# Kernel optimization log

Measured on AMD Instinct MI355X. Metric: run time of the kernel, lower is better.

## Reference

```python
import jax, jax.numpy as jnp
import numpy as np

# DSCNPair config (init_kwargs)
C = 256          # d_model
G = 16           # group
K = 3            # kernel_size
DW = 3           # dw_kernel_size
PAD = 1
STRIDE = 1
DIL = 1
GC = C // G      # group_channels
P = K * K        # sampling points per group
OFFSET_SCALE = 1.0
B, H, W = 8, 64, 64


def _dwconv(x, w, b, pad):
    # depthwise conv: x (N,C,H,W), w (C,1,kh,kw)
    out = jax.lax.conv_general_dilated(
        x, w, (1, 1), [(pad, pad), (pad, pad)],
        dimension_numbers=('NCHW', 'OIHW', 'NCHW'), feature_group_count=x.shape[1])
    return out + b[None, :, None, None]


def _dcn_core(x, offset, mask):
    # x: (N,H,W,C) NHWC; offset: (N,H,W,G*P*2); mask: (N,H,W,G*P) already softmaxed per group
    N, Hh, Ww, _ = x.shape
    xp = jnp.pad(x, ((0, 0), (PAD, PAD), (PAD, PAD), (0, 0)))
    Hp, Wp = Hh + 2 * PAD, Ww + 2 * PAD
    Ho = (Hp - (DIL * (K - 1) + 1)) // STRIDE + 1
    Wo = (Wp - (DIL * (K - 1) + 1)) // STRIDE + 1
    # reference points (normalized by padded spatial size)
    base = (DIL * (K - 1)) // 2 + 0.5
    ref_y = (base + jnp.arange(Ho, dtype=x.dtype) * STRIDE) / Hp
    ref_x = (base + jnp.arange(Wo, dtype=x.dtype) * STRIDE) / Wp
    # dilation grid, kw-major ordering to match torch.meshgrid(lin_w, lin_h) in DCNv3
    pts = -((DIL * (K - 1)) // 2) + jnp.arange(K, dtype=x.dtype) * DIL
    gx = jnp.repeat(pts, K) / Wp
    gy = jnp.tile(pts, K) / Hp
    off = offset.reshape(N, Ho, Wo, G, P, 2) * (OFFSET_SCALE / jnp.array([Wp, Hp], x.dtype))
    loc_x = ref_x[None, None, :, None, None] + OFFSET_SCALE * gx + off[..., 0]  # (N,Ho,Wo,G,P)
    loc_y = ref_y[None, :, None, None, None] + OFFSET_SCALE * gy + off[..., 1]
    # grid_sample(bilinear, padding_mode='zeros', align_corners=False):
    # grid g = 2*loc-1; unnormalized idx = ((g+1)*size - 1)/2 = loc*size - 0.5
    ix = loc_x * Wp - 0.5
    iy = loc_y * Hp - 0.5
    x0 = jnp.floor(ix)
    y0 = jnp.floor(iy)
    xg = xp.reshape(N, Hp, Wp, G, GC)
    n_idx = jnp.arange(N)[:, None, None, None, None]
    g_idx = jnp.arange(G)[None, None, None, :, None]

    def gather(yi, xi):
        valid = ((yi >= 0) & (yi < Hp) & (xi >= 0) & (xi < Wp)).astype(x.dtype)
        yc = jnp.clip(yi, 0, Hp - 1).astype(jnp.int32)
        xc = jnp.clip(xi, 0, Wp - 1).astype(jnp.int32)
        return xg[n_idx, yc, xc, g_idx] * valid[..., None]  # (N,Ho,Wo,G,P,GC)

    wx1 = ix - x0; wx0 = 1.0 - wx1
    wy1 = iy - y0; wy0 = 1.0 - wy1
    out = (gather(y0, x0) * (wy0 * wx0)[..., None]
           + gather(y0, x0 + 1) * (wy0 * wx1)[..., None]
           + gather(y0 + 1, x0) * (wy1 * wx0)[..., None]
           + gather(y0 + 1, x0 + 1) * (wy1 * wx1)[..., None])
    out = (out * mask.reshape(N, Ho, Wo, G, P, 1)).sum(4)   # (N,Ho,Wo,G,GC)
    return out.reshape(N, Ho, Wo, G * GC)


def _forward(x, conv0_w, conv0_b, dw_w, dw_b, ln_g, ln_b, off_w, off_b,
             msk_w, msk_b, in_w, in_b, outp_w, outp_b, pw_w, pw_b):
    u = x
    h = _dwconv(x, conv0_w, conv0_b, 2)             # 5x5 depthwise, pad 2
    inp = jnp.transpose(h, (0, 2, 3, 1))            # NHWC, input to DCNv3
    xproj = inp @ in_w + in_b                       # input_proj
    # dw_conv branch: depthwise conv -> LayerNorm(channels_last) -> GELU
    x1 = _dwconv(jnp.transpose(inp, (0, 3, 1, 2)), dw_w, dw_b, (DW - 1) // 2)
    x1 = jnp.transpose(x1, (0, 2, 3, 1))
    mu = x1.mean(-1, keepdims=True)
    var = jnp.mean((x1 - mu) ** 2, -1, keepdims=True)
    x1 = (x1 - mu) * jax.lax.rsqrt(var + 1e-5) * ln_g + ln_b
    x1 = jax.nn.gelu(x1, approximate=False)
    offset = x1 @ off_w + off_b                     # (B,H,W,G*P*2)
    m = jax.nn.softmax((x1 @ msk_w + msk_b).reshape(B, H, W, G, P), axis=-1)
    m = m.reshape(B, H, W, G * P)
    y = _dcn_core(xproj, offset, m)
    y = y @ outp_w + outp_b                         # output_proj
    attn = jnp.einsum('nhwc,dc->ndhw', y, pw_w) + pw_b[None, :, None, None]  # 1x1 conv
    return u * attn


def setup_inputs() -> dict:
    key = jax.random.key(0)
    ks = jax.random.split(key, 8)
    s = 0.05
    return {
        'x': jax.random.normal(ks[0], (B, C, H, W), jnp.float32),
        'conv0_w': jax.random.normal(ks[1], (C, 1, 5, 5), jnp.float32) * s,
        'conv0_b': jnp.zeros((C,), jnp.float32),
        'dw_w': jax.random.normal(ks[2], (C, 1, DW, DW), jnp.float32) * s,
        'dw_b': jnp.zeros((C,), jnp.float32),
        'ln_g': jnp.ones((C,), jnp.float32),
        'ln_b': jnp.zeros((C,), jnp.float32),
        'off_w': jax.random.normal(ks[3], (C, G * P * 2), jnp.float32) * s,
        'off_b': jnp.zeros((G * P * 2,), jnp.float32),
        'msk_w': jax.random.normal(ks[4], (C, G * P), jnp.float32) * s,
        'msk_b': jnp.zeros((G * P,), jnp.float32),
        'in_w': jax.random.normal(ks[5], (C, C), jnp.float32) * s,
        'in_b': jnp.zeros((C,), jnp.float32),
        'outp_w': jax.random.normal(ks[6], (C, C), jnp.float32) * s,
        'outp_b': jnp.zeros((C,), jnp.float32),
        'pw_w': jax.random.normal(ks[7], (C, C), jnp.float32) * s,
        'pw_b': jnp.zeros((C,), jnp.float32),
    }


def reference(x, conv0_w, conv0_b, dw_w, dw_b, ln_g, ln_b, off_w, off_b,
              msk_w, msk_b, in_w, in_b, outp_w, outp_b, pw_w, pw_b):
    return _forward(x, conv0_w, conv0_b, dw_w, dw_b, ln_g, ln_b, off_w, off_b,
                    msk_w, msk_b, in_w, in_b, outp_w, outp_b, pw_w, pw_b)
```

## Files before the change

kernel.cpp:

```cpp
#include <hip/hip_runtime.h>
#include <hip/hip_bf16.h>
#include <hip/hip_fp16.h>
#include <math.h>

#define BB 8
#define CC 256
#define HH 64
#define WW 64
#define GG 16
#define GCH 16
#define PP 9
#define NPIX (BB*HH*WW)

typedef __attribute__((ext_vector_type(4))) float f32x4;
typedef __bf16 bf16x8 __attribute__((ext_vector_type(8)));

#define GLOAD_LDS16(g, l) __builtin_amdgcn_global_load_lds( \
    (const __attribute__((address_space(1))) unsigned int*)(g), \
    (__attribute__((address_space(3))) unsigned int*)(l), 16, 0, 0)

__device__ __forceinline__ void bfu2(unsigned a, float& lo, float& hi) {
    union { unsigned u; float f; } t0, t1;
    t0.u = a << 16; t1.u = a & 0xffff0000u;
    lo = t0.f; hi = t1.f;
}

#define C0PLANE 817
__global__ void conv0_kernel(const float* __restrict__ x, const float* __restrict__ w,
                             const float* __restrict__ b,
                             __hip_bfloat16* __restrict__ out_bf) {
    __shared__ float sx[16 * C0PLANE];
    int t  = threadIdx.x;
    int st = blockIdx.x;
    int cg = blockIdx.y;
    int n  = blockIdx.z;
    int h0 = st * 8;
    int c0 = cg * 16;

    #pragma unroll
    for (int i = 0; i < 12; ++i) {
        int task = i * 256 + t;
        int lane = task & 15;
        int pair = task >> 4;
        int c    = pair / 12;
        int row  = pair - c * 12;
        int gy   = h0 - 2 + row;
        float4 v = make_float4(0.f, 0.f, 0.f, 0.f);
        if (gy >= 0 && gy < HH)
            v = *(const float4*)(x + (((size_t)(n * CC + c0 + c)) * HH + gy) * WW + lane * 4);
        *(float4*)&sx[c * C0PLANE + row * 68 + 2 + lane * 4] = v;
    }
    if (t < 192) {
        int c = t / 12, row = t - (t / 12) * 12;
        float* p = &sx[c * C0PLANE + row * 68];
        p[0] = 0.f; p[1] = 0.f; p[66] = 0.f; p[67] = 0.f;
    }
    __syncthreads();

    int c = t & 15;
    int s = t >> 4;
    float wreg[25];
    const float* wp = w + (c0 + c) * 25;
    #pragma unroll
    for (int i = 0; i < 25; ++i) wreg[i] = wp[i];
    float bias = b[c0 + c];
    const float* cp = &sx[c * C0PLANE + s * 4];

    float win[5][8];
    #pragma unroll
    for (int rr = 0; rr < 4; ++rr)
        #pragma unroll
        for (int j = 0; j < 8; ++j) win[rr][j] = cp[rr * 68 + j];

    #pragma unroll
    for (int r = 0; r < 8; ++r) {
        #pragma unroll
        for (int j = 0; j < 8; ++j) win[(r + 4) % 5][j] = cp[(r + 4) * 68 + j];
        float a0 = bias, a1 = bias, a2 = bias, a3 = bias;
        #pragma unroll
        for (int dy = 0; dy < 5; ++dy) {
            const float* wr = &wreg[dy * 5];
            const float* wd = win[(r + dy) % 5];
            #pragma unroll
            for (int dx = 0; dx < 5; ++dx) {
                float wv = wr[dx];
                a0 += wd[0 + dx] * wv;
                a1 += wd[1 + dx] * wv;
                a2 += wd[2 + dx] * wv;
                a3 += wd[3 + dx] * wv;
            }
        }
        size_t pixb = ((size_t)n * 4096 + (h0 + r) * 64 + s * 4) << 8;
        out_bf[pixb + c0 + c]       = __float2bfloat16(a0);
        out_bf[pixb + 256 + c0 + c] = __float2bfloat16(a1);
        out_bf[pixb + 512 + c0 + c] = __float2bfloat16(a2);
        out_bf[pixb + 768 + c0 + c] = __float2bfloat16(a3);
    }
}

__global__ void dwln_kernel(const __hip_bfloat16* __restrict__ inp, const float* __restrict__ dww,
                            const float* __restrict__ dwb, const float* __restrict__ lng,
                            const float* __restrict__ lnb, __hip_bfloat16* __restrict__ x1) {
    __shared__ float sx[3 * 10 * 256];
    __shared__ float ls1[8][4], ls2[8][4];
    int t  = threadIdx.x;
    int x0 = blockIdx.x * 8;
    int h  = blockIdx.y;
    int n  = blockIdx.z;

    #pragma unroll
    for (int i = 0; i < 4; ++i) {
        int task = i * 256 + t;
        if (task < 960) {
            int c8  = task & 31;
            int rem = task >> 5;
            int r   = rem / 10;
            int xx  = rem - r * 10;
            int gy = h + r - 1, gx = x0 + xx - 1;
            float4 A = make_float4(0.f,0.f,0.f,0.f), B = make_float4(0.f,0.f,0.f,0.f);
            if (gy >= 0 && gy < HH && gx >= 0 && gx < WW) {
                uint4 u = *(const uint4*)(inp + (((size_t)(n * HH + gy)) * WW + gx) * CC + c8 * 8);
                bfu2(u.x, A.x, A.y); bfu2(u.y, A.z, A.w);
                bfu2(u.z, B.x, B.y); bfu2(u.w, B.z, B.w);
            }
            *(float4*)&sx[(r * 10 + xx) * 256 + c8 * 8]     = A;
            *(float4*)&sx[(r * 10 + xx) * 256 + c8 * 8 + 4] = B;
        }
    }
    __syncthreads();

    int c = t;
    float wr[9];
    #pragma unroll
    for (int i = 0; i < 9; ++i) wr[i] = dww[c * 9 + i];
    float bias = dwb[c];
    float a[8];
    #pragma unroll
    for (int px = 0; px < 8; ++px) {
        float acc = bias;
        #pragma unroll
        for (int dy = 0; dy < 3; ++dy)
            #pragma unroll
            for (int dx = 0; dx < 3; ++dx)
                acc += sx[(dy * 10 + px + dx) * 256 + c] * wr[dy * 3 + dx];
        a[px] = acc;
    }

    int wid = t >> 6, lane = t & 63;
    #pragma unroll
    for (int px = 0; px < 8; ++px) {
        float s1 = a[px], s2 = a[px] * a[px];
        #pragma unroll
        for (int o = 1; o < 64; o <<= 1) {
            s1 += __shfl_xor(s1, o);
            s2 += __shfl_xor(s2, o);
        }
        if (lane == 0) { ls1[px][wid] = s1; ls2[px][wid] = s2; }
    }
    __syncthreads();

    float gam = lng[c], bet = lnb[c];
    #pragma unroll
    for (int px = 0; px < 8; ++px) {
        float t1 = ls1[px][0] + ls1[px][1] + ls1[px][2] + ls1[px][3];
        float t2 = ls2[px][0] + ls2[px][1] + ls2[px][2] + ls2[px][3];
        float mu  = t1 * (1.0f/256.0f);
        float var = t2 * (1.0f/256.0f) - mu * mu;
        float rr  = rsqrtf(var + 1e-5f);
        float v = (a[px] - mu) * rr * gam + bet;
        float g = 0.5f * v * (1.0f + erff(v * 0.70710678118654752440f));
        x1[(((size_t)(n * HH + h)) * WW + x0 + px) * CC + c] = __float2bfloat16(g);
    }
}

__global__ void wcvt_t_kernel(const float* __restrict__ W, __hip_bfloat16* __restrict__ Bt, int N) {
    int idx = blockIdx.x * 256 + threadIdx.x;
    int n = idx >> 8, k = idx & 255;
    float v = (n < N) ? W[k * N + n] : 0.0f;
    Bt[idx] = __float2bfloat16(v);
}
__global__ void wcomb_kernel(const float* __restrict__ outpw, const float* __restrict__ pww,
                             __hip_bfloat16* __restrict__ Wc) {
    __shared__ float pd[256];
    int d = blockIdx.x, k = threadIdx.x;
    pd[k] = pww[d * 256 + k];
    __syncthreads();
    const float* ow = outpw + k * 256;
    float s = 0.0f;
    #pragma unroll 8
    for (int c = 0; c < 256; ++c) s += ow[c] * pd[c];
    Wc[d * 256 + k] = __float2bfloat16(s);
}
__global__ void bcomb_kernel(const float* __restrict__ outpb, const float* __restrict__ pww,
                             const float* __restrict__ pwb, float* __restrict__ bc) {
    int d = threadIdx.x;
    const float* pr = pww + d * 256;
    float s = pwb[d];
    #pragma unroll 8
    for (int c = 0; c < 256; ++c) s += outpb[c] * pr[c];
    bc[d] = s;
}

__device__ __forceinline__ void stage_tile(const __hip_bfloat16* __restrict__ A,
                                           const __hip_bfloat16* __restrict__ Bt,
                                           __bf16* As, __bf16* Bs,
                                           int bm, int bn, int k0, int w, int l) {
    #pragma unroll
    for (int i = 0; i < 4; ++i) {
        int q = w*256 + i*64 + l;
        int row = q >> 3, sk = q & 7;
        const __hip_bfloat16* g = A + (((size_t)(bm + row)) << 8) + k0 + sk*8;
        GLOAD_LDS16(g, As + (w*256 + i*64)*8);
    }
    #pragma unroll
    for (int i = 0; i < 2; ++i) {
        int q = w*128 + i*64 + l;
        int row = q >> 3, sk = q & 7;
        const __hip_bfloat16* g = Bt + (((size_t)(bn + row)) << 8) + k0 + sk*8;
        GLOAD_LDS16(g, Bs + (w*128 + i*64)*8);
    }
}

template <int OUT_BF16, int NBOUND>
__global__ void mgemm_kernel(const __hip_bfloat16* __restrict__ A,
                             const __hip_bfloat16* __restrict__ Bt,
                             const float* __restrict__ bias,
                             void* __restrict__ Cout, int N, int ldc) {
    __shared__ __bf16 smem[24576];
    int tid = threadIdx.x;
    int w = tid >> 6, l = tid & 63;
    int bn = blockIdx.x * 64;
    int bm = blockIdx.y * 128;
    __bf16* Asb[2] = { smem,        smem + 12288 };
    __bf16* Bsb[2] = { smem + 8192, smem + 20480 };
    f32x4 acc[2][4];
    #pragma unroll
    for (int m = 0; m < 2; ++m)
        #pragma unroll
        for (int n = 0; n < 4; ++n)
            acc[m][n] = (f32x4){0.f, 0.f, 0.f, 0.f};

    stage_tile(A, Bt, Asb[0], Bsb[0], bm, bn, 0, w, l);
    __syncthreads();
    int lr = l & 15, kg = l >> 4;
    #pragma unroll
    for (int t = 0; t < 4; ++t) {
        int cur = t & 1;
        if (t < 3) stage_tile(A, Bt, Asb[cur^1], Bsb[cur^1], bm, bn, (t+1)*64, w, l);
        const __bf16* Ab = Asb[cur];
        const __bf16* Bb = Bsb[cur];
        bf16x8 af[2][2], bfr[4][2];
        #pragma unroll
        for (int m = 0; m < 2; ++m)
            #pragma unroll
            for (int u = 0; u < 2; ++u)
                af[m][u] = *(const bf16x8*)&Ab[(w*32 + m*16 + lr)*64 + u*32 + kg*8];
        #pragma unroll
        for (int n = 0; n < 4; ++n)
            #pragma unroll
            for (int u = 0; u < 2; ++u)
                bfr[n][u] = *(const bf16x8*)&Bb[(n*16 + lr)*64 + u*32 + kg*8];
        #pragma unroll
        for (int u = 0; u < 2; ++u)
            #pragma unroll
            for (int m = 0; m < 2; ++m)
                #pragma unroll
                for (int n = 0; n < 4; ++n)
                    acc[m][n] = __builtin_amdgcn_mfma_f32_16x16x32_bf16(af[m][u], bfr[n][u], acc[m][n], 0, 0, 0);
        __syncthreads();
    }
    int orow = bm + w*32 + kg*4;
    #pragma unroll
    for (int n = 0; n < 4; ++n) {
        int ccol = bn + n*16 + lr;
        if (NBOUND && ccol >= N) continue;
        float bv = bias[ccol];
        #pragma unroll
        for (int m = 0; m < 2; ++m) {
            #pragma unroll
            for (int j = 0; j < 4; ++j) {
                size_t o = (size_t)(orow + m*16 + j) * ldc + ccol;
                float v = acc[m][n][j] + bv;
                if (OUT_BF16) ((__hip_bfloat16*)Cout)[o] = __float2bfloat16(v);
                else          ((float*)Cout)[o] = v;
            }
        }
    }
}

__global__ void dcn_kernel(const __hip_bfloat16* __restrict__ xproj,
                           const __hip_bfloat16* __restrict__ off,
                           const __hip_bfloat16* __restrict__ mlog,
                           __hip_bfloat16* __restrict__ y) {
    __shared__ uint2 wLds[1152];
    __shared__ int   oLds[1152];
    int pix0 = blockIdx.x * 8;
    int t = threadIdx.x;

    if (t < 128) {
        int px = t >> 4;
        int g  = t & 15;
        int pix = pix0 + px;
        int wo = pix & 63, ho = (pix >> 6) & 63;
        const __hip_bfloat16* mb = mlog + (size_t)pix * 144 + g * 9;
        float lg[9];
        float mx = -1e30f;
        #pragma unroll
        for (int p = 0; p < 9; ++p) { lg[p] = __bfloat162float(mb[p]); mx = fmaxf(mx, lg[p]); }
        float se = 0.f;
        #pragma unroll
        for (int p = 0; p < 9; ++p) { lg[p] = __expf(lg[p] - mx); se += lg[p]; }
        float rs = 1.0f / se;
        const unsigned* ob = (const unsigned*)(off + (size_t)pix * 288 + g * 18);
        #pragma unroll
        for (int p = 0; p < 9; ++p) {
            float ox, oy;
            bfu2(ob[p], ox, oy);
            float m = lg[p] * rs;
            int dx = p / 3 - 1;
            int dy = p - (p / 3) * 3 - 1;
            float fx = (float)(wo + dx) + ox;
            float fy = (float)(ho + dy) + oy;
            float x0f = floorf(fx), y0f = floorf(fy);
            int x0 = (int)x0f, y0 = (int)y0f;
            int x1 = x0 + 1, y1 = y0 + 1;
            float wx1 = fx - x0f, wx0 = 1.0f - wx1;
            float wy1 = fy - y0f, wy0 = 1.0f - wy1;
            float vx0 = (x0 >= 0 && x0 < WW) ? 1.0f : 0.0f;
            float vx1 = (x1 >= 0 && x1 < WW) ? 1.0f : 0.0f;
            float vy0 = (y0 >= 0 && y0 < HH) ? 1.0f : 0.0f;
            float vy1 = (y1 >= 0 && y1 < HH) ? 1.0f : 0.0f;
            int x0c = min(max(x0, 0), WW - 1), x1c = min(max(x1, 0), WW - 1);
            int y0c = min(max(y0, 0), HH - 1), y1c = min(max(y1, 0), HH - 1);
            int tau = px * 144 + g * 9 + p;
            union { __half2 h2; unsigned u; } pa, pb;
            pa.h2 = __floats2half2_rn(m * wy0 * wx0 * vy0 * vx0,
                                      m * wy0 * wx1 * vy0 * vx1);
            pb.h2 = __floats2half2_rn(m * wy1 * wx0 * vy1 * vx0,
                                      m * wy1 * wx1 * vy1 * vx1);
            wLds[tau] = make_uint2(pa.u, pb.u);
            oLds[tau] = (y0c * WW + x0c) | ((x1c - x0c) << 12) | ((y1c - y0c) << 13);
        }
    }
    __syncthreads();

    int px = t >> 5;
    int l  = t & 31;
    int g  = l >> 1;
    int ch = g * 16 + (l & 1) * 8;
    int pix = pix0 + px;
    int n = pix >> 12;
    const __hip_bfloat16* xb = xproj + ((size_t)n << 20) + ch;
    float a0=0,a1=0,a2=0,a3=0,a4=0,a5=0,a6=0,a7=0;
    const uint2* wp = &wLds[px * 144 + g * 9];
    const int*   op = &oLds[px * 144 + g * 9];
    #pragma unroll
    for (int p = 0; p < 9; ++p) {
        uint2 pw = wp[p];
        union { unsigned u; __half2 h2; } ua, ub;
        ua.u = pw.x; ub.u = pw.y;
        float2 fA = __half22float2(ua.h2);
        float2 fB = __half22float2(ub.h2);
        float w00 = fA.x, w01 = fA.y, w10 = fB.x, w11 = fB.y;
        int pk = op[p];
        int base = (pk & 4095) << 8;
        int ddx  = ((pk >> 12) & 1) << 8;
        int ddy  = ((pk >> 13) & 1) << 14;
        {
            uint4 u = *(const uint4*)(xb + base);
            float b0,b1,b2,b3,b4,b5,b6,b7;
            bfu2(u.x,b0,b1); bfu2(u.y,b2,b3); bfu2(u.z,b4,b5); bfu2(u.w,b6,b7);
            a0 += w00*b0; a1 += w00*b1; a2 += w00*b2; a3 += w00*b3;
            a4 += w00*b4; a5 += w00*b5; a6 += w00*b6; a7 += w00*b7;
        }
        {
            uint4 u = *(const uint4*)(xb + base + ddx);
            float b0,b1,b2,b3,b4,b5,b6,b7;
            bfu2(u.x,b0,b1); bfu2(u.y,b2,b3); bfu2(u.z,b4,b5); bfu2(u.w,b6,b7);
            a0 += w01*b0; a1 += w01*b1; a2 += w01*b2; a3 += w01*b3;
            a4 += w01*b4; a5 += w01*b5; a6 += w01*b6; a7 += w01*b7;
        }
        {
            uint4 u = *(const uint4*)(xb + base + ddy);
            float b0,b1,b2,b3,b4,b5,b6,b7;
            bfu2(u.x,b0,b1); bfu2(u.y,b2,b3); bfu2(u.z,b4,b5); bfu2(u.w,b6,b7);
            a0 += w10*b0; a1 += w10*b1; a2 += w10*b2; a3 += w10*b3;
            a4 += w10*b4; a5 += w10*b5; a6 += w10*b6; a7 += w10*b7;
        }
        {
            uint4 u = *(const uint4*)(xb + base + ddy + ddx);
            float b0,b1,b2,b3,b4,b5,b6,b7;
            bfu2(u.x,b0,b1); bfu2(u.y,b2,b3); bfu2(u.z,b4,b5); bfu2(u.w,b6,b7);
            a0 += w11*b0; a1 += w11*b1; a2 += w11*b2; a3 += w11*b3;
            a4 += w11*b4; a5 += w11*b5; a6 += w11*b6; a7 += w11*b7;
        }
    }
    union { __hip_bfloat16 h[8]; uint4 u; } ov;
    ov.h[0]=__float2bfloat16(a0); ov.h[1]=__float2bfloat16(a1);
    ov.h[2]=__float2bfloat16(a2); ov.h[3]=__float2bfloat16(a3);
    ov.h[4]=__float2bfloat16(a4); ov.h[5]=__float2bfloat16(a5);
    ov.h[6]=__float2bfloat16(a6); ov.h[7]=__float2bfloat16(a7);
    *(uint4*)(y + (size_t)pix * CC + ch) = ov.u;
}

__global__ void finmul_kernel(const float* __restrict__ x, const __hip_bfloat16* __restrict__ attn,
                              float* __restrict__ out) {
    __shared__ float t[16][17];
    int pix0 = blockIdx.x * 16;
    int d0   = blockIdx.y * 16;
    int li = threadIdx.x & 15;
    int lj = threadIdx.x >> 4;
    t[lj][li] = __bfloat162float(attn[(size_t)(pix0 + lj)*CC + d0 + li]);
    __syncthreads();
    int pix = pix0 + li;
    int wo = pix & 63;
    int ho = (pix >> 6) & 63;
    int n  = pix >> 12;
    int d = d0 + lj;
    size_t oidx = (((size_t)n*CC + d)*HH + ho)*WW + wo;
    out[oidx] = x[oidx] * t[li][lj];
}

extern "C" void kernel_launch(void* const* d_in, const int* in_sizes, int n_in,
                              void* d_out, int out_size, void* d_ws, size_t ws_size,
                              hipStream_t stream) {
    const float* x      = (const float*)d_in[0];
    const float* conv0w = (const float*)d_in[1];
    const float* conv0b = (const float*)d_in[2];
    const float* dww    = (const float*)d_in[3];
    const float* dwb    = (const float*)d_in[4];
    const float* lng    = (const float*)d_in[5];
    const float* lnb    = (const float*)d_in[6];
    const float* offw   = (const float*)d_in[7];
    const float* offb   = (const float*)d_in[8];
    const float* mskw   = (const float*)d_in[9];
    const float* mskb   = (const float*)d_in[10];
    const float* inw    = (const float*)d_in[11];
    const float* inb    = (const float*)d_in[12];
    const float* outpw  = (const float*)d_in[13];
    const float* outpb  = (const float*)d_in[14];
    const float* pww    = (const float*)d_in[15];
    const float* pwb    = (const float*)d_in[16];

    __hip_bfloat16* bfb = (__hip_bfloat16*)d_ws;
    __hip_bfloat16* inp_bf  = bfb;
    __hip_bfloat16* y_bf    = inp_bf;
    __hip_bfloat16* x1_bf   = bfb + 8388608;
    __hip_bfloat16* xpj_bf  = x1_bf;
    __hip_bfloat16* attn_bf = x1_bf;
    __hip_bfloat16* off_bf  = bfb + 16777216;
    __hip_bfloat16* msk_bf  = bfb + 26214400;
    __hip_bfloat16* bt_in   = bfb + 30932992;
    __hip_bfloat16* bt_off  = bt_in  + 65536;
    __hip_bfloat16* bt_msk  = bt_off + 81920;
    __hip_bfloat16* bt_wc   = bt_msk + 49152;
    float* bcomb = (float*)(bt_wc + 65536);
    float* out = (float*)d_out;

    wcvt_t_kernel<<<256, 256, 0, stream>>>(inw,  bt_in,  256);
    wcvt_t_kernel<<<320, 256, 0, stream>>>(offw, bt_off, 288);
    wcvt_t_kernel<<<192, 256, 0, stream>>>(mskw, bt_msk, 144);
    wcomb_kernel<<<256, 256, 0, stream>>>(outpw, pww, bt_wc);
    bcomb_kernel<<<1, 256, 0, stream>>>(outpb, pww, pwb, bcomb);

    conv0_kernel<<<dim3(8, 16, BB), 256, 0, stream>>>(x, conv0w, conv0b, inp_bf);
    dwln_kernel<<<dim3(8, 64, BB), 256, 0, stream>>>(inp_bf, dww, dwb, lng, lnb, x1_bf);
    mgemm_kernel<1,1><<<dim3(5, 256), 256, 0, stream>>>(x1_bf, bt_off, offb, off_bf, 288, 288);
    mgemm_kernel<1,1><<<dim3(3, 256), 256, 0, stream>>>(x1_bf, bt_msk, mskb, msk_bf, 144, 144);
    mgemm_kernel<1,0><<<dim3(4, 256), 256, 0, stream>>>(inp_bf, bt_in, inb, xpj_bf, 256, 256);
    dcn_kernel<<<NPIX/8, 256, 0, stream>>>(xpj_bf, off_bf, msk_bf, y_bf);
    mgemm_kernel<1,0><<<dim3(4, 256), 256, 0, stream>>>(y_bf, bt_wc, bcomb, attn_bf, 256, 256);
    finmul_kernel<<<dim3(NPIX/16, 16), 256, 0, stream>>>(x, attn_bf, out);
}
```

Baseline: 192.3 us.

## Fuse final attention GEMM with elementwise multiply and remap DCN block order

The last projection GEMM now stages its output tile in LDS as fp32, transposes it, and multiplies it directly by x in NCHW layout, writing the final output. This removes the bf16 attention intermediate and the separate finmul kernel, along with its strided transposed accesses. The DCN kernel also permutes its block index so that concurrently running blocks cover spread-out pixel ranges, which changes the cache and channel access pattern. The fused epilogue uses padded LDS (stride 133) and float4 global loads and stores, and it keeps the product in fp32 instead of rounding attention to bf16.

Measured after the change: 185.2 us. 3.7% less time.

```diff
diff --git a/kernel.cpp b/kernel.cpp
--- a/kernel.cpp
+++ b/kernel.cpp
@@ -221,11 +221,11 @@
     }
 }
 
-template <int OUT_BF16, int NBOUND>
+template <int NBOUND>
 __global__ void mgemm_kernel(const __hip_bfloat16* __restrict__ A,
                              const __hip_bfloat16* __restrict__ Bt,
                              const float* __restrict__ bias,
-                             void* __restrict__ Cout, int N, int ldc) {
+                             __hip_bfloat16* __restrict__ Cout, int N, int ldc) {
     __shared__ __bf16 smem[24576];
     int tid = threadIdx.x;
     int w = tid >> 6, l = tid & 63;
@@ -280,11 +280,93 @@
             #pragma unroll
             for (int j = 0; j < 4; ++j) {
                 size_t o = (size_t)(orow + m*16 + j) * ldc + ccol;
-                float v = acc[m][n][j] + bv;
-                if (OUT_BF16) ((__hip_bfloat16*)Cout)[o] = __float2bfloat16(v);
-                else          ((float*)Cout)[o] = v;
+                Cout[o] = __float2bfloat16(acc[m][n][j] + bv);
             }
         }
+    }
+}
+
+__global__ void attn_fused_kernel(const __hip_bfloat16* __restrict__ A,
+                                  const __hip_bfloat16* __restrict__ Bt,
+                                  const float* __restrict__ bias,
+                                  const float* __restrict__ x,
+                                  float* __restrict__ out) {
+    __shared__ __bf16 smem[24576];
+    int tid = threadIdx.x;
+    int w = tid >> 6, l = tid & 63;
+    int bn = blockIdx.x * 64;
+    int bm = blockIdx.y * 128;
+    __bf16* Asb[2] = { smem,        smem + 12288 };
+    __bf16* Bsb[2] = { smem + 8192, smem + 20480 };
+    f32x4 acc[2][4];
+    #pragma unroll
+    for (int m = 0; m < 2; ++m)
+        #pragma unroll
+        for (int n = 0; n < 4; ++n)
+            acc[m][n] = (f32x4){0.f, 0.f, 0.f, 0.f};
+
+    stage_tile(A, Bt, Asb[0], Bsb[0], bm, bn, 0, w, l);
+    __syncthreads();
+    int lr = l & 15, kg = l >> 4;
+    #pragma unroll
+    for (int t = 0; t < 4; ++t) {
+        int cur = t & 1;
+        if (t < 3) stage_tile(A, Bt, Asb[cur^1], Bsb[cur^1], bm, bn, (t+1)*64, w, l);
+        const __bf16* Ab = Asb[cur];
+        const __bf16* Bb = Bsb[cur];
+        bf16x8 af[2][2], bfr[4][2];
+        #pragma unroll
+        for (int m = 0; m < 2; ++m)
+            #pragma unroll
+            for (int u = 0; u < 2; ++u)
+                af[m][u] = *(const bf16x8*)&Ab[(w*32 + m*16 + lr)*64 + u*32 + kg*8];
+        #pragma unroll
+        for (int n = 0; n < 4; ++n)
+            #pragma unroll
+            for (int u = 0; u < 2; ++u)
+                bfr[n][u] = *(const bf16x8*)&Bb[(n*16 + lr)*64 + u*32 + kg*8];
+        #pragma unroll
+        for (int u = 0; u < 2; ++u)
+            #pragma unroll
+            for (int m = 0; m < 2; ++m)
+                #pragma unroll
+                for (int n = 0; n < 4; ++n)
+                    acc[m][n] = __builtin_amdgcn_mfma_f32_16x16x32_bf16(af[m][u], bfr[n][u], acc[m][n], 0, 0, 0);
+        __syncthreads();
+    }
+
+    float* cLds = (float*)smem;
+    int rel0 = w*32 + kg*4;
+    #pragma unroll
+    for (int n = 0; n < 4; ++n) {
+        int col = n*16 + lr;
+        float bv = bias[bn + col];
+        #pragma unroll
+        for (int m = 0; m < 2; ++m) {
+            #pragma unroll
+            for (int j = 0; j < 4; ++j)
+                cLds[col * 133 + rel0 + m*16 + j] = acc[m][n][j] + bv;
+        }
+    }
+    __syncthreads();
+
+    int d  = tid >> 2;
+    int po = (tid & 3) * 32;
+    int n_img = bm >> 12;
+    int rem   = bm & 4095;
+    size_t gb = (((size_t)(n_img * CC + bn + d)) << 12) + rem + po;
+    const float* xr = x + gb;
+    float* ow = out + gb;
+    const float* cr = &cLds[d * 133 + po];
+    #pragma unroll
+    for (int j = 0; j < 32; j += 4) {
+        float4 xv = *(const float4*)(xr + j);
+        float4 r;
+        r.x = xv.x * cr[j+0];
+        r.y = xv.y * cr[j+1];
+        r.z = xv.z * cr[j+2];
+        r.w = xv.w * cr[j+3];
+        *(float4*)(ow + j) = r;
     }
 }
 
@@ -294,7 +376,9 @@
                            __hip_bfloat16* __restrict__ y) {
     __shared__ uint2 wLds[1152];
     __shared__ int   oLds[1152];
-    int pix0 = blockIdx.x * 8;
+    int bid = blockIdx.x;
+    int blk = (bid & 7) * 512 + (bid >> 3);
+    int pix0 = blk * 8;
     int t = threadIdx.x;
 
     if (t < 128) {
@@ -403,24 +487,6 @@
     *(uint4*)(y + (size_t)pix * CC + ch) = ov.u;
 }
 
-__global__ void finmul_kernel(const float* __restrict__ x, const __hip_bfloat16* __restrict__ attn,
-                              float* __restrict__ out) {
-    __shared__ float t[16][17];
-    int pix0 = blockIdx.x * 16;
-    int d0   = blockIdx.y * 16;
-    int li = threadIdx.x & 15;
-    int lj = threadIdx.x >> 4;
-    t[lj][li] = __bfloat162float(attn[(size_t)(pix0 + lj)*CC + d0 + li]);
-    __syncthreads();
-    int pix = pix0 + li;
-    int wo = pix & 63;
-    int ho = (pix >> 6) & 63;
-    int n  = pix >> 12;
-    int d = d0 + lj;
-    size_t oidx = (((size_t)n*CC + d)*HH + ho)*WW + wo;
-    out[oidx] = x[oidx] * t[li][lj];
-}
-
 extern "C" void kernel_launch(void* const* d_in, const int* in_sizes, int n_in,
                               void* d_out, int out_size, void* d_ws, size_t ws_size,
                               hipStream_t stream) {
@@ -447,7 +513,6 @@
     __hip_bfloat16* y_bf    = inp_bf;
     __hip_bfloat16* x1_bf   = bfb + 8388608;
     __hip_bfloat16* xpj_bf  = x1_bf;
-    __hip_bfloat16* attn_bf = x1_bf;
     __hip_bfloat16* off_bf  = bfb + 16777216;
     __hip_bfloat16* msk_bf  = bfb + 26214400;
     __hip_bfloat16* bt_in   = bfb + 30932992;
@@ -465,10 +530,9 @@
 
     conv0_kernel<<<dim3(8, 16, BB), 256, 0, stream>>>(x, conv0w, conv0b, inp_bf);
     dwln_kernel<<<dim3(8, 64, BB), 256, 0, stream>>>(inp_bf, dww, dwb, lng, lnb, x1_bf);
-    mgemm_kernel<1,1><<<dim3(5, 256), 256, 0, stream>>>(x1_bf, bt_off, offb, off_bf, 288, 288);
-    mgemm_kernel<1,1><<<dim3(3, 256), 256, 0, stream>>>(x1_bf, bt_msk, mskb, msk_bf, 144, 144);
-    mgemm_kernel<1,0><<<dim3(4, 256), 256, 0, stream>>>(inp_bf, bt_in, inb, xpj_bf, 256, 256);
+    mgemm_kernel<1><<<dim3(5, 256), 256, 0, stream>>>(x1_bf, bt_off, offb, off_bf, 288, 288);
+    mgemm_kernel<1><<<dim3(3, 256), 256, 0, stream>>>(x1_bf, bt_msk, mskb, msk_bf, 144, 144);
+    mgemm_kernel<0><<<dim3(4, 256), 256, 0, stream>>>(inp_bf, bt_in, inb, xpj_bf, 256, 256);
     dcn_kernel<<<NPIX/8, 256, 0, stream>>>(xpj_bf, off_bf, msk_bf, y_bf);
-    mgemm_kernel<1,0><<<dim3(4, 256), 256, 0, stream>>>(y_bf, bt_wc, bcomb, attn_bf, 256, 256);
-    finmul_kernel<<<dim3(NPIX/16, 16), 256, 0, stream>>>(x, attn_bf, out);
-}
+    attn_fused_kernel<<<dim3(4, 256), 256, 0, stream>>>(y_bf, bt_wc, bcomb, x, out);
+}
```
